# Kernel tuning notes

Measured on AMD Instinct MI355X. Metric: run time of the kernel, lower is better.

The kernel has to match this reference:

```python
import jax, jax.numpy as jnp
import numpy as np

N = 100000   # nodes
E = 640000   # edges
IN = 256     # raw input feature dim
D = 128      # post-MLP node feature dim (fixed in FilterGNN)


def setup_inputs() -> dict:
    key = jax.random.key(0)
    ks = jax.random.split(key, 10)
    x = jax.random.normal(ks[0], (N, IN), jnp.float32)
    alpha = jax.random.uniform(ks[1], (E, 1), jnp.float32)  # edge gate logits in [0,1)
    edge_index = jax.random.randint(ks[2], (2, E), 0, N, dtype=jnp.int32)
    norm = jnp.ones((E,), jnp.float32)  # passed to message in the original but unused
    # MLP `lin`: in_channels -> 512 -> 256 -> 128 (kaiming-normal weights, zero bias)
    def kaiming(k, fan_out, fan_in):
        return jax.random.normal(k, (fan_out, fan_in), jnp.float32) * jnp.sqrt(2.0 / fan_in)
    W1 = kaiming(ks[3], 512, IN); b1 = jnp.zeros((512,), jnp.float32)
    W2 = kaiming(ks[4], 256, 512); b2 = jnp.zeros((256,), jnp.float32)
    W3 = kaiming(ks[5], D, 256);  b3 = jnp.zeros((D,), jnp.float32)
    return {"x": x, "alpha": alpha, "edge_index": edge_index, "norm": norm,
            "W1": W1, "b1": b1, "W2": W2, "b2": b2, "W3": W3, "b3": b3}


def reference(x, alpha, edge_index, norm, W1, b1, W2, b2, W3, b3):
    # FilterGNN.lin: Linear-Tanh-Linear-Tanh-Linear  -> [N, 128]
    h = jnp.tanh(x @ W1.T + b1)
    h = jnp.tanh(h @ W2.T + b2)
    h = h @ W3.T + b3
    # FilterGraphConv1: gather x_j, elementwise relu gate, scatter-mean over targets.
    # (The [-1, H, C] view with H*C = 128 is a pure reshape; the gate broadcasts
    #  over all features, so the math is identical without the head split.)
    src, dst = edge_index[0], edge_index[1]
    gate = 2.0 * jax.nn.relu(jax.lax.stop_gradient(alpha) - 0.5)  # [E, 1]
    msg = h[src] * gate                                           # [E, 128] gather + gate
    sums = jax.ops.segment_sum(msg, dst, num_segments=N)          # [N, 128]
    cnt = jax.ops.segment_sum(jnp.ones((E,), h.dtype), dst, num_segments=N)
    out = sums / jnp.maximum(cnt, 1.0)[:, None]                   # scatter-mean (0 if no edges)
    return out
```

## Files before the change

kernel.cpp:

```cpp
#include <hip/hip_runtime.h>

typedef __attribute__((ext_vector_type(8))) short short8;
typedef __attribute__((ext_vector_type(4))) float f32x4;

__device__ __forceinline__ unsigned short f2bf(float f) {
    union { float f; unsigned u; } v; v.f = f;
    unsigned r = v.u + 0x7FFFu + ((v.u >> 16) & 1u);
    return (unsigned short)(r >> 16);
}
__device__ __forceinline__ float bf2f(unsigned short h) {
    union { unsigned u; float f; } v; v.u = ((unsigned)h) << 16;
    return v.f;
}

__device__ __forceinline__ float tanh_fast(float x) {
    float xc = fminf(fmaxf(x, -9.0f), 9.0f);
    float t  = __expf(2.0f * xc);
    return (t - 1.0f) * __builtin_amdgcn_rcpf(t + 1.0f);
}

#define GLD16(gptr, lptr)                                                     \
    __builtin_amdgcn_global_load_lds(                                         \
        (const __attribute__((address_space(1))) unsigned int*)(gptr),        \
        (__attribute__((address_space(3))) unsigned int*)(lptr), 16, 0, 0)

__global__ __launch_bounds__(256) void cast_all(
    const float* __restrict__ x,  unsigned short* __restrict__ xbf,
    const float* __restrict__ W1, unsigned short* __restrict__ w1bf,
    const float* __restrict__ W2, unsigned short* __restrict__ w2bf,
    const float* __restrict__ W3, unsigned short* __restrict__ w3bf,
    int xq)
{
    int t = blockIdx.x * 256 + threadIdx.x;
    const float* s; unsigned short* d; int q;
    if (t < xq) { s = x; d = xbf; q = t; }
    else {
        int u = t - xq;
        if (u < 32768)      { s = W1; d = w1bf; q = u; }
        else if (u < 65536) { s = W2; d = w2bf; q = u - 32768; }
        else if (u < 73728) { s = W3; d = w3bf; q = u - 65536; }
        else return;
    }
    int base = q * 4;
    float4 v = *(const float4*)(s + base);
    unsigned long long p =
        (unsigned long long)f2bf(v.x)
      | ((unsigned long long)f2bf(v.y) << 16)
      | ((unsigned long long)f2bf(v.z) << 32)
      | ((unsigned long long)f2bf(v.w) << 48);
    *(unsigned long long*)(d + base) = p;
}

#define TM 128
#define TN 128
#define BK 64

__global__ __launch_bounds__(256) void gemm_bt(
    const unsigned short* __restrict__ A, const unsigned short* __restrict__ B,
    const float* __restrict__ bias, unsigned short* __restrict__ C,
    int M, int N, int K)
{
    __shared__ __align__(16) short As[TM][BK];
    __shared__ __align__(16) short Bs[TM][BK];

    const int g  = blockIdx.x;
    const int bx = (g >> 5) * 8 + (g & 7);
    const int by = (g >> 3) & 3;
    const int mblk = (M + TM - 1) / TM;
    if (bx >= mblk) return;

    const int tid  = threadIdx.x;
    const int wave = tid >> 6;
    const int lane = tid & 63;
    const int m0 = bx * TM;
    const int n0 = by * TN;
    const int wm = (wave >> 1) * 64;
    const int wn = (wave & 1) * 64;
    const int lm = lane & 15;
    const int quad = lane >> 4;

    const int srow = lane >> 3;
    const int scol = ((lane & 7) ^ srow) * 8;
    const int cc0 = (quad ^ (lm & 7)) * 8;
    const int cc1 = ((4 + quad) ^ (lm & 7)) * 8;

    f32x4 acc[4][4] = {};

    for (int k0 = 0; k0 < K; k0 += BK) {
        #pragma unroll
        for (int i = 0; i < 4; ++i) {
            int row = wave * 32 + i * 8;
            int gr = m0 + row + srow; if (gr >= M) gr = M - 1;
            GLD16(A + (size_t)gr * K + k0 + scol, &As[row][0]);
            GLD16(B + (size_t)(n0 + row + srow) * K + k0 + scol, &Bs[row][0]);
        }
        __syncthreads();

        #pragma unroll
        for (int ks = 0; ks < BK; ks += 32) {
            const int cc = (ks == 0) ? cc0 : cc1;
            short8 af[4], bf_[4];
            #pragma unroll
            for (int i = 0; i < 4; ++i) {
                af[i]  = *(const short8*)&As[wm + i * 16 + lm][cc];
                bf_[i] = *(const short8*)&Bs[wn + i * 16 + lm][cc];
            }
            #pragma unroll
            for (int im = 0; im < 4; ++im)
                #pragma unroll
                for (int in = 0; in < 4; ++in)
                    acc[im][in] = __builtin_amdgcn_mfma_f32_16x16x32_bf16(
                        af[im], bf_[in], acc[im][in], 0, 0, 0);
        }
        __syncthreads();
    }

    #pragma unroll
    for (int im = 0; im < 4; ++im) {
        int gm_base = m0 + wm + im * 16 + quad * 4;
        #pragma unroll
        for (int in = 0; in < 4; ++in) {
            int gn = n0 + wn + in * 16 + lm;
            float bv = bias[gn];
            #pragma unroll
            for (int r = 0; r < 4; ++r) {
                int gm = gm_base + r;
                if (gm < M) {
                    float v = tanh_fast(acc[im][in][r] + bv);
                    C[(size_t)gm * N + gn] = f2bf(v);
                }
            }
        }
    }
}

__global__ __launch_bounds__(256) void gemm23_hist(
    const unsigned short* __restrict__ h1, const unsigned short* __restrict__ W2,
    const float* __restrict__ b2, const unsigned short* __restrict__ W3,
    const float* __restrict__ b3, unsigned short* __restrict__ hout, int M,
    const int* __restrict__ ei, const float* __restrict__ alpha,
    unsigned long long* __restrict__ deg, int E, int gblk)
{
    __shared__ __align__(16) short pool[16896 + 128 * 64];
    short (*As)[64]  = (short(*)[64])pool;
    short (*Bs)[64]  = (short(*)[64])(pool + 4096);
    short (*h2s)[264] = (short(*)[264])pool;
    short (*Bs3)[64] = (short(*)[64])(pool + 16896);

    if ((int)blockIdx.x >= gblk) {
        int e = (blockIdx.x - gblk) * 256 + threadIdx.x;
        if (e < E) {
            int dst = ei[E + e];
            float gate = 2.0f * fmaxf(alpha[e] - 0.5f, 0.0f);
            atomicAdd(&deg[dst], 0x100000000ULL | (gate > 0.0f ? 1ULL : 0ULL));
        }
        return;
    }

    const int tid  = threadIdx.x;
    const int wave = tid >> 6;
    const int lane = tid & 63;
    const int m0 = blockIdx.x * 64;
    const int wm = (wave >> 1) * 32;
    const int lm = lane & 15;
    const int quad = lane >> 4;
    const int srow = lane >> 3;
    const int scol = ((lane & 7) ^ srow) * 8;
    const int cc0 = (quad ^ (lm & 7)) * 8;
    const int cc1 = ((4 + quad) ^ (lm & 7)) * 8;

    {
        const int wn = (wave & 1) * 128;
        f32x4 acc[2][8] = {};
        for (int k0 = 0; k0 < 512; k0 += 64) {
            #pragma unroll
            for (int i = 0; i < 2; ++i) {
                int r0 = wave * 16 + i * 8;
                int gr = m0 + r0 + srow; if (gr >= M) gr = M - 1;
                GLD16(h1 + (size_t)gr * 512 + k0 + scol, &As[r0][0]);
            }
            #pragma unroll
            for (int i = 0; i < 8; ++i) {
                int r0 = wave * 64 + i * 8;
                GLD16(W2 + (size_t)(r0 + srow) * 512 + k0 + scol, &Bs[r0][0]);
            }
            __syncthreads();
            #pragma unroll
            for (int ks = 0; ks < 64; ks += 32) {
                const int cc = (ks == 0) ? cc0 : cc1;
                short8 af[2], bf_[8];
                #pragma unroll
                for (int i = 0; i < 2; ++i) af[i]  = *(const short8*)&As[wm + i * 16 + lm][cc];
                #pragma unroll
                for (int i = 0; i < 8; ++i) bf_[i] = *(const short8*)&Bs[wn + i * 16 + lm][cc];
                #pragma unroll
                for (int im = 0; im < 2; ++im)
                    #pragma unroll
                    for (int in = 0; in < 8; ++in)
                        acc[im][in] = __builtin_amdgcn_mfma_f32_16x16x32_bf16(
                            af[im], bf_[in], acc[im][in], 0, 0, 0);
            }
            __syncthreads();
        }
        #pragma unroll
        for (int im = 0; im < 2; ++im) {
            int rb = wm + im * 16 + quad * 4;
            #pragma unroll
            for (int in = 0; in < 8; ++in) {
                int col = wn + in * 16 + lm;
                float bv = b2[col];
                #pragma unroll
                for (int r = 0; r < 4; ++r)
                    h2s[rb + r][col] = (short)f2bf(tanh_fast(acc[im][in][r] + bv));
            }
        }
    }
    __syncthreads();

    {
        const int wn = (wave & 1) * 64;
        f32x4 acc[2][4] = {};
        for (int k0 = 0; k0 < 256; k0 += 64) {
            #pragma unroll
            for (int i = 0; i < 4; ++i) {
                int r0 = wave * 32 + i * 8;
                GLD16(W3 + (size_t)(r0 + srow) * 256 + k0 + scol, &Bs3[r0][0]);
            }
            __syncthreads();
            #pragma unroll
            for (int ks = 0; ks < 64; ks += 32) {
                const int cc = (ks == 0) ? cc0 : cc1;
                short8 af[2], bf_[4];
                #pragma unroll
                for (int i = 0; i < 2; ++i)
                    af[i] = *(const short8*)&h2s[wm + i * 16 + lm][k0 + ks + quad * 8];
                #pragma unroll
                for (int i = 0; i < 4; ++i)
                    bf_[i] = *(const short8*)&Bs3[wn + i * 16 + lm][cc];
                #pragma unroll
                for (int im = 0; im < 2; ++im)
                    #pragma unroll
                    for (int in = 0; in < 4; ++in)
                        acc[im][in] = __builtin_amdgcn_mfma_f32_16x16x32_bf16(
                            af[im], bf_[in], acc[im][in], 0, 0, 0);
            }
            __syncthreads();
        }
        #pragma unroll
        for (int im = 0; im < 2; ++im) {
            int gm_base = m0 + wm + im * 16 + quad * 4;
            #pragma unroll
            for (int in = 0; in < 4; ++in) {
                int gn = wn + in * 16 + lm;
                float bv = b3[gn];
                #pragma unroll
                for (int r = 0; r < 4; ++r) {
                    int gm = gm_base + r;
                    if (gm < M)
                        hout[(size_t)gm * 128 + gn] = f2bf(acc[im][in][r] + bv);
                }
            }
        }
    }
}

__global__ __launch_bounds__(256) void scan1(
    const unsigned long long* __restrict__ deg, int* __restrict__ rowptr,
    int* __restrict__ cursor, int* __restrict__ gcounter, int N)
{
    __shared__ int sums[256];
    __shared__ int base_sh;
    int base = blockIdx.x * 1024 + threadIdx.x * 4;
    int v[4];
    #pragma unroll
    for (int i = 0; i < 4; ++i) {
        int idx = base + i;
        v[i] = (idx < N) ? (int)(deg[idx] & 0xffffffffULL) : 0;
    }
    int s = v[0] + v[1] + v[2] + v[3];
    sums[threadIdx.x] = s;
    __syncthreads();
    for (int off = 1; off < 256; off <<= 1) {
        int t = (threadIdx.x >= off) ? sums[threadIdx.x - off] : 0;
        __syncthreads();
        sums[threadIdx.x] += t;
        __syncthreads();
    }
    int excl = sums[threadIdx.x] - s;
    if (threadIdx.x == 255) base_sh = atomicAdd(gcounter, sums[255]);
    __syncthreads();
    int run = base_sh + excl;
    #pragma unroll
    for (int i = 0; i < 4; ++i) {
        int idx = base + i;
        if (idx < N) { rowptr[idx] = run; cursor[idx] = run; }
        run += v[i];
    }
}

__global__ __launch_bounds__(256) void edge_fill(
    const int* __restrict__ ei, const float* __restrict__ alpha,
    int* __restrict__ cursor, int2* __restrict__ recs, int E)
{
    int e = blockIdx.x * 256 + threadIdx.x;
    if (e >= E) return;
    float gate = 2.0f * fmaxf(alpha[e] - 0.5f, 0.0f);
    if (gate > 0.0f) {
        int dst = ei[E + e];
        int src = ei[e];
        int pos = atomicAdd(&cursor[dst], 1);
        recs[pos] = make_int2(src, __float_as_int(gate));
    }
}

__global__ __launch_bounds__(256) void node_gather(
    const unsigned short* __restrict__ h, const unsigned long long* __restrict__ deg,
    const int* __restrict__ rowptr, const int2* __restrict__ recs,
    float* __restrict__ out, int N)
{
    int wave = threadIdx.x >> 6;
    int lane = threadIdx.x & 63;
    int node = blockIdx.x * 4 + wave;
    if (node >= N) return;
    unsigned long long d = deg[node];
    int dAll  = __builtin_amdgcn_readfirstlane((int)(d >> 32));
    int dG    = __builtin_amdgcn_readfirstlane((int)(d & 0xffffffffULL));
    int start = __builtin_amdgcn_readfirstlane(rowptr[node]);
    int qw = lane >> 4, ql = lane & 15;
    float a[8] = {};
    for (int j = 0; j < dG; j += 4) {
        int jj = j + qw;
        int idx = start + (jj < dG ? jj : dG - 1);
        int2 rec = recs[idx];
        float gate = (jj < dG) ? __int_as_float(rec.y) : 0.0f;
        uint4 u = *(const uint4*)(h + ((size_t)rec.x << 7) + ql * 8);
        a[0] += bf2f((unsigned short)(u.x & 0xffffu)) * gate;
        a[1] += bf2f((unsigned short)(u.x >> 16)) * gate;
        a[2] += bf2f((unsigned short)(u.y & 0xffffu)) * gate;
        a[3] += bf2f((unsigned short)(u.y >> 16)) * gate;
        a[4] += bf2f((unsigned short)(u.z & 0xffffu)) * gate;
        a[5] += bf2f((unsigned short)(u.z >> 16)) * gate;
        a[6] += bf2f((unsigned short)(u.w & 0xffffu)) * gate;
        a[7] += bf2f((unsigned short)(u.w >> 16)) * gate;
    }
    #pragma unroll
    for (int i = 0; i < 8; ++i) {
        a[i] += __shfl_xor(a[i], 16);
        a[i] += __shfl_xor(a[i], 32);
    }
    if (qw == 0) {
        float inv = 1.0f / fmaxf((float)dAll, 1.0f);
        float* op = out + ((size_t)node << 7) + ql * 8;
        *(float4*)(op)     = make_float4(a[0] * inv, a[1] * inv, a[2] * inv, a[3] * inv);
        *(float4*)(op + 4) = make_float4(a[4] * inv, a[5] * inv, a[6] * inv, a[7] * inv);
    }
}

extern "C" void kernel_launch(void* const* d_in, const int* in_sizes, int n_in,
                              void* d_out, int out_size, void* d_ws, size_t ws_size,
                              hipStream_t stream) {
    const float* x     = (const float*)d_in[0];
    const float* alpha = (const float*)d_in[1];
    const int*   ei    = (const int*)d_in[2];
    const float* W1 = (const float*)d_in[4];
    const float* b1 = (const float*)d_in[5];
    const float* W2 = (const float*)d_in[6];
    const float* b2 = (const float*)d_in[7];
    const float* W3 = (const float*)d_in[8];
    const float* b3 = (const float*)d_in[9];
    float* out = (float*)d_out;

    const int N = in_sizes[0] / 256;
    const int E = in_sizes[1];
    const int IN = 256, H1 = 512, D = 128;

    char* ws = (char*)d_ws;
    size_t off = 0;
    auto take = [&](size_t bytes) { char* p = ws + off; off = (off + bytes + 255) & ~(size_t)255; return p; };
    unsigned short* xbf  = (unsigned short*)take((size_t)N * IN * 2);
    unsigned short* h1bf = (unsigned short*)take((size_t)N * H1 * 2);
    unsigned short* hbf  = (unsigned short*)take((size_t)N * D  * 2);
    unsigned short* w1bf = (unsigned short*)take((size_t)H1 * IN * 2);
    unsigned short* w2bf = (unsigned short*)take((size_t)256 * H1 * 2);
    unsigned short* w3bf = (unsigned short*)take((size_t)D * 256 * 2);

    char* cbase = (char*)xbf;
    size_t coff = 0;
    auto ctake = [&](size_t bytes) { char* p = cbase + coff; coff = (coff + bytes + 255) & ~(size_t)255; return p; };
    unsigned long long* deg = (unsigned long long*)ctake((size_t)N * 8);
    int*  gcounter = (int*)ctake(256);
    int*  rowptr   = (int*)ctake((size_t)N * 4);
    int*  cursor   = (int*)ctake((size_t)N * 4);
    int2* recs     = (int2*)ctake((size_t)E * 8);

    dim3 blk(256);

    const int xq = N * IN / 4;
    const int castN = xq + 73728;
    cast_all<<<(castN + 255) / 256, blk, 0, stream>>>(x, xbf, W1, w1bf, W2, w2bf, W3, w3bf, xq);

    const int mblk = (N + TM - 1) / TM;
    const int g1 = ((mblk + 7) / 8) * 32;
    gemm_bt<<<dim3(g1), blk, 0, stream>>>(xbf, w1bf, b1, h1bf, N, H1, IN);

    hipMemsetAsync(deg, 0, (size_t)N * 8 + 256, stream);
    const int gblk = (N + 63) / 64;
    const int eblk = (E + 255) / 256;
    gemm23_hist<<<gblk + eblk, blk, 0, stream>>>(
        h1bf, w2bf, b2, w3bf, b3, hbf, N, ei, alpha, deg, E, gblk);

    const int nb1 = (N + 1023) / 1024;
    scan1<<<nb1, blk, 0, stream>>>(deg, rowptr, cursor, gcounter, N);
    edge_fill<<<eblk, blk, 0, stream>>>(ei, alpha, cursor, recs, E);

    node_gather<<<(N + 3) / 4, blk, 0, stream>>>(hbf, deg, rowptr, recs, out, N);
}
```

Before: 386.3 us.

## Fuse x fp32-to-bf16 cast into first GEMM's A-tile load

Removes the separate pass that converts the whole x matrix to bf16. The first GEMM now reads fp32 x directly, packs it to bf16 in registers and stores it into swizzled LDS, while the weight cast shrinks to a small kernel. This drops a full write and re-read of the bf16 copy of x. The cost is that each of the four N-column blocks re-reads fp32 x, which is twice the bytes of bf16. A-tile loading also moves from async global_load_lds to register-staged loads, which may reduce latency hiding. Scratch buffers no longer alias the xbf region, and the LDS pool in gemm23 is split into separate arrays, which increases its shared memory use.

```diff
diff --git a/kernel.cpp b/kernel.cpp
--- a/kernel.cpp
+++ b/kernel.cpp
@@ -19,36 +19,32 @@
     return (t - 1.0f) * __builtin_amdgcn_rcpf(t + 1.0f);
 }
 
+__device__ __forceinline__ unsigned long long pack4(float4 v) {
+    return (unsigned long long)f2bf(v.x)
+         | ((unsigned long long)f2bf(v.y) << 16)
+         | ((unsigned long long)f2bf(v.z) << 32)
+         | ((unsigned long long)f2bf(v.w) << 48);
+}
+
 #define GLD16(gptr, lptr)                                                     \
     __builtin_amdgcn_global_load_lds(                                         \
         (const __attribute__((address_space(1))) unsigned int*)(gptr),        \
         (__attribute__((address_space(3))) unsigned int*)(lptr), 16, 0, 0)
 
-__global__ __launch_bounds__(256) void cast_all(
-    const float* __restrict__ x,  unsigned short* __restrict__ xbf,
+__global__ __launch_bounds__(256) void cast_w(
     const float* __restrict__ W1, unsigned short* __restrict__ w1bf,
     const float* __restrict__ W2, unsigned short* __restrict__ w2bf,
-    const float* __restrict__ W3, unsigned short* __restrict__ w3bf,
-    int xq)
+    const float* __restrict__ W3, unsigned short* __restrict__ w3bf)
 {
     int t = blockIdx.x * 256 + threadIdx.x;
     const float* s; unsigned short* d; int q;
-    if (t < xq) { s = x; d = xbf; q = t; }
-    else {
-        int u = t - xq;
-        if (u < 32768)      { s = W1; d = w1bf; q = u; }
-        else if (u < 65536) { s = W2; d = w2bf; q = u - 32768; }
-        else if (u < 73728) { s = W3; d = w3bf; q = u - 65536; }
-        else return;
-    }
+    if (t < 32768)      { s = W1; d = w1bf; q = t; }
+    else if (t < 65536) { s = W2; d = w2bf; q = t - 32768; }
+    else if (t < 73728) { s = W3; d = w3bf; q = t - 65536; }
+    else return;
     int base = q * 4;
     float4 v = *(const float4*)(s + base);
-    unsigned long long p =
-        (unsigned long long)f2bf(v.x)
-      | ((unsigned long long)f2bf(v.y) << 16)
-      | ((unsigned long long)f2bf(v.z) << 32)
-      | ((unsigned long long)f2bf(v.w) << 48);
-    *(unsigned long long*)(d + base) = p;
+    *(unsigned long long*)(d + base) = pack4(v);
 }
 
 #define TM 128
@@ -56,7 +52,7 @@
 #define BK 64
 
 __global__ __launch_bounds__(256) void gemm_bt(
-    const unsigned short* __restrict__ A, const unsigned short* __restrict__ B,
+    const float* __restrict__ x, const unsigned short* __restrict__ B,
     const float* __restrict__ bias, unsigned short* __restrict__ C,
     int M, int N, int K)
 {
@@ -84,14 +80,26 @@
     const int cc0 = (quad ^ (lm & 7)) * 8;
     const int cc1 = ((4 + quad) ^ (lm & 7)) * 8;
 
+    const int ac  = tid & 7;
+    const int arb = tid >> 3;
+
     f32x4 acc[4][4] = {};
 
     for (int k0 = 0; k0 < K; k0 += BK) {
+        #pragma unroll
+        for (int j = 0; j < 4; ++j) {
+            int r = arb + j * 32;
+            int gr = m0 + r; if (gr >= M) gr = M - 1;
+            const float* p = x + (size_t)gr * K + k0 + ac * 8;
+            float4 a0 = *(const float4*)(p);
+            float4 a1 = *(const float4*)(p + 4);
+            unsigned long long* d =
+                (unsigned long long*)&As[r][(ac ^ (r & 7)) * 8];
+            d[0] = pack4(a0); d[1] = pack4(a1);
+        }
         #pragma unroll
         for (int i = 0; i < 4; ++i) {
             int row = wave * 32 + i * 8;
-            int gr = m0 + row + srow; if (gr >= M) gr = M - 1;
-            GLD16(A + (size_t)gr * K + k0 + scol, &As[row][0]);
             GLD16(B + (size_t)(n0 + row + srow) * K + k0 + scol, &Bs[row][0]);
         }
         __syncthreads();
@@ -141,11 +149,9 @@
     const int* __restrict__ ei, const float* __restrict__ alpha,
     unsigned long long* __restrict__ deg, int E, int gblk)
 {
-    __shared__ __align__(16) short pool[16896 + 128 * 64];
-    short (*As)[64]  = (short(*)[64])pool;
-    short (*Bs)[64]  = (short(*)[64])(pool + 4096);
-    short (*h2s)[264] = (short(*)[264])pool;
-    short (*Bs3)[64] = (short(*)[64])(pool + 16896);
+    __shared__ __align__(16) short As[64][64];
+    __shared__ __align__(16) short Bs[256][64];
+    __shared__ __align__(16) short h2s[64][264];
 
     if ((int)blockIdx.x >= gblk) {
         int e = (blockIdx.x - gblk) * 256 + threadIdx.x;
@@ -219,6 +225,7 @@
 
     {
         const int wn = (wave & 1) * 64;
+        short (*Bs3)[64] = (short(*)[64])&Bs[0][0];
         f32x4 acc[2][4] = {};
         for (int k0 = 0; k0 < 256; k0 += 64) {
             #pragma unroll
@@ -377,33 +384,27 @@
     char* ws = (char*)d_ws;
     size_t off = 0;
     auto take = [&](size_t bytes) { char* p = ws + off; off = (off + bytes + 255) & ~(size_t)255; return p; };
-    unsigned short* xbf  = (unsigned short*)take((size_t)N * IN * 2);
     unsigned short* h1bf = (unsigned short*)take((size_t)N * H1 * 2);
     unsigned short* hbf  = (unsigned short*)take((size_t)N * D  * 2);
     unsigned short* w1bf = (unsigned short*)take((size_t)H1 * IN * 2);
     unsigned short* w2bf = (unsigned short*)take((size_t)256 * H1 * 2);
     unsigned short* w3bf = (unsigned short*)take((size_t)D * 256 * 2);
-
-    char* cbase = (char*)xbf;
-    size_t coff = 0;
-    auto ctake = [&](size_t bytes) { char* p = cbase + coff; coff = (coff + bytes + 255) & ~(size_t)255; return p; };
-    unsigned long long* deg = (unsigned long long*)ctake((size_t)N * 8);
-    int*  gcounter = (int*)ctake(256);
-    int*  rowptr   = (int*)ctake((size_t)N * 4);
-    int*  cursor   = (int*)ctake((size_t)N * 4);
-    int2* recs     = (int2*)ctake((size_t)E * 8);
+    unsigned long long* deg = (unsigned long long*)take((size_t)N * 8);
+    int*  gcounter = (int*)take(256);
+    int*  rowptr   = (int*)take((size_t)N * 4);
+    int*  cursor   = (int*)take((size_t)N * 4);
+    int2* recs     = (int2*)take((size_t)E * 8);
 
     dim3 blk(256);
 
-    const int xq = N * IN / 4;
-    const int castN = xq + 73728;
-    cast_all<<<(castN + 255) / 256, blk, 0, stream>>>(x, xbf, W1, w1bf, W2, w2bf, W3, w3bf, xq);
+    hipMemsetAsync(deg, 0, (size_t)N * 8 + 256, stream);
+
+    cast_w<<<288, blk, 0, stream>>>(W1, w1bf, W2, w2bf, W3, w3bf);
 
     const int mblk = (N + TM - 1) / TM;
     const int g1 = ((mblk + 7) / 8) * 32;
-    gemm_bt<<<dim3(g1), blk, 0, stream>>>(xbf, w1bf, b1, h1bf, N, H1, IN);
-
-    hipMemsetAsync(deg, 0, (size_t)N * 8 + 256, stream);
+    gemm_bt<<<dim3(g1), blk, 0, stream>>>(x, w1bf, b1, h1bf, N, H1, IN);
+
     const int gblk = (N + 63) / 64;
     const int eblk = (E + 255) / 256;
     gemm23_hist<<<gblk + eblk, blk, 0, stream>>>(
```

New measurement: 411.6 us. 6.5% more time.
